# Optimization experiments

Measured on AMD Instinct MI355X. Metric: run time of the kernel, lower is better.

## Reference

```python
import jax, jax.numpy as jnp
import numpy as np

B, D_IN = 4096, 1024
E, K = 16, 2
EMB = 256
H1, H2 = 2048, 1024  # hidden_units, hidden_units // 2
O = 512              # num_classes


def setup_inputs() -> dict:
    key = jax.random.key(0)
    ks = jax.random.split(key, 10)
    s = lambda *sh: 1.0 / np.sqrt(sh[-2] if len(sh) > 1 else 1.0)
    return {
        "x":   jax.random.normal(ks[0], (B, D_IN), jnp.float32),
        "Wr":  jax.random.normal(ks[1], (D_IN, EMB), jnp.float32) * (1.0 / np.sqrt(D_IN)),
        "br":  jnp.zeros((EMB,), jnp.float32),
        "emb": jax.random.normal(ks[2], (E, EMB), jnp.float32) * (1.0 / np.sqrt(EMB)),
        "W1":  jax.random.normal(ks[3], (E, D_IN, H1), jnp.float32) * (1.0 / np.sqrt(D_IN)),
        "b1":  jnp.zeros((E, H1), jnp.float32),
        "W2":  jax.random.normal(ks[4], (E, H1, H2), jnp.float32) * (1.0 / np.sqrt(H1)),
        "b2":  jnp.zeros((E, H2), jnp.float32),
        "W3":  jax.random.normal(ks[5], (E, H2, O), jnp.float32) * (1.0 / np.sqrt(H2)),
        "b3":  jnp.zeros((E, O), jnp.float32),
    }


def reference(x, Wr, br, emb, W1, b1, W2, b2, W3, b3):
    # Router query: [B, EMB]
    q = x @ Wr + br
    # Negative squared euclidean distance to expert embeddings -> scores [B, E]
    d2 = jnp.sum(jnp.square(q[:, None, :] - emb[None, :, :]), axis=-1)
    scores = -d2
    gating_probs = jax.nn.softmax(scores, axis=-1)  # [B, E]
    # Top-k selection + renormalized gates
    top_v, top_i = jax.lax.top_k(scores, K)          # [B, K]
    gates = jax.nn.softmax(top_v, axis=-1)           # [B, K]
    # All experts run on full batch (dense), batched over expert axis
    h1 = jax.nn.relu(jnp.einsum('bi,eih->beh', x, W1) + b1)   # [B, E, H1]
    h2 = jax.nn.relu(jnp.einsum('beh,ehm->bem', h1, W2) + b2)  # [B, E, H2]
    out = jnp.einsum('bem,emo->beo', h2, W3) + b3              # [B, E, O]
    # Gather top-k expert outputs per example and combine
    sel = jnp.take_along_axis(out, top_i[:, :, None], axis=1)  # [B, K, O]
    final = jnp.sum(sel * gates[:, :, None], axis=1)           # [B, O]
    return final, q, gating_probs
```

## Files before the change

### kernel.cpp

```cpp
#include <hip/hip_runtime.h>
#include <hip/hip_bf16.h>

using bf16 = __hip_bfloat16;
typedef __attribute__((ext_vector_type(8))) short bf16x8;
typedef __attribute__((ext_vector_type(8))) unsigned short u16x8;
typedef __attribute__((ext_vector_type(4))) float f32x4;

constexpr int BATCH = 4096;
constexpr int D_IN  = 1024;
constexpr int NEXP  = 16;
constexpr int EMB   = 256;
constexpr int H1    = 2048;
constexpr int H2    = 1024;
constexpr int OUTD  = 512;
constexpr int SLOTS = BATCH * 2;
constexpr int SLOTS_PAD = SLOTS + 256;
constexpr int MAX_T128 = SLOTS / 128 + NEXP;
constexpr int K3    = 3 * D_IN;

constexpr size_t WS_XB     = 0;
constexpr size_t WS_XLO    = WS_XB     + (size_t)BATCH * D_IN * 2;
constexpr size_t WS_H1     = WS_XLO    + (size_t)BATCH * D_IN * 2;
constexpr size_t WS_H2     = WS_H1     + (size_t)SLOTS_PAD * H1 * 2;
constexpr size_t WS_OSL    = WS_H2     + (size_t)SLOTS_PAD * H2 * 2;
constexpr size_t WS_TOPI   = WS_OSL    + (size_t)SLOTS_PAD * OUTD * 4;
constexpr size_t WS_GATES  = WS_TOPI   + (size_t)SLOTS * 4;
constexpr size_t WS_SLOTOF = WS_GATES  + (size_t)SLOTS * 4;
constexpr size_t WS_TOKL   = WS_SLOTOF + (size_t)SLOTS * 4;
constexpr size_t WS_CNT    = WS_TOKL   + (size_t)SLOTS_PAD * 4;
constexpr size_t WS_TMAP   = WS_CNT    + 64 * 4;
constexpr size_t WS_WR3    = ((WS_TMAP + (size_t)MAX_T128 * 8) + 255) & ~(size_t)255;
constexpr size_t WS_WT     = ((WS_WR3 + (size_t)EMB * K3 * 2) + 255) & ~(size_t)255;

__device__ __forceinline__ unsigned short f2bf(float f) {
    bf16 h = __float2bfloat16(f);
    return __builtin_bit_cast(unsigned short, h);
}
__device__ __forceinline__ float bf2f(unsigned short h) {
    return __builtin_bit_cast(float, (unsigned)h << 16);
}

__device__ __forceinline__ void gload16(const unsigned short* g, unsigned short* l) {
    __builtin_amdgcn_global_load_lds(
        (const __attribute__((address_space(1))) unsigned int*)g,
        (__attribute__((address_space(3))) unsigned int*)l, 16, 0, 0);
}

template <int N>
__device__ __forceinline__ void waitcnt_vm() {
    if constexpr (N == 0)       asm volatile("s_waitcnt vmcnt(0)" ::: "memory");
    else if constexpr (N == 4)  asm volatile("s_waitcnt vmcnt(4)" ::: "memory");
    else if constexpr (N == 6)  asm volatile("s_waitcnt vmcnt(6)" ::: "memory");
    else if constexpr (N == 8)  asm volatile("s_waitcnt vmcnt(8)" ::: "memory");
    else if constexpr (N == 12) asm volatile("s_waitcnt vmcnt(12)" ::: "memory");
    else if constexpr (N == 16) asm volatile("s_waitcnt vmcnt(16)" ::: "memory");
    else static_assert(N == 0, "add case");
}

__global__ __launch_bounds__(256) void k_cvt_x(const float* __restrict__ x,
                                               unsigned short* __restrict__ xhi,
                                               unsigned short* __restrict__ xlo) {
    int i = blockIdx.x * 256 + threadIdx.x;
    float4 v = reinterpret_cast<const float4*>(x)[i];
    ushort4 h, l;
    h.x = f2bf(v.x); h.y = f2bf(v.y); h.z = f2bf(v.z); h.w = f2bf(v.w);
    l.x = f2bf(v.x - bf2f(h.x)); l.y = f2bf(v.y - bf2f(h.y));
    l.z = f2bf(v.z - bf2f(h.z)); l.w = f2bf(v.w - bf2f(h.w));
    reinterpret_cast<ushort4*>(xhi)[i] = h;
    reinterpret_cast<ushort4*>(xlo)[i] = l;
}

__global__ __launch_bounds__(256) void k_wr3(const float* __restrict__ Wr,
                                             unsigned short* __restrict__ Wrt3) {
    __shared__ float Tf[64][65];
    int n0 = blockIdx.x * 64, k0 = blockIdx.y * 64;
    const float* Wb = Wr + (size_t)k0 * EMB + n0;
    int t  = threadIdx.x;
    int kr = t >> 4, c4 = (t & 15) * 4;
#pragma unroll
    for (int i = 0; i < 4; i++) {
        float4 v = *reinterpret_cast<const float4*>(Wb + (size_t)(kr + i * 16) * EMB + c4);
        Tf[kr + i * 16][c4 + 0] = v.x; Tf[kr + i * 16][c4 + 1] = v.y;
        Tf[kr + i * 16][c4 + 2] = v.z; Tf[kr + i * 16][c4 + 3] = v.w;
    }
    __syncthreads();
#pragma unroll
    for (int i = 0; i < 2; i++) {
        int idx = t + i * 256;
        int n = idx >> 3, ck = (idx & 7) * 8;
        u16x8 hi, lo;
#pragma unroll
        for (int j = 0; j < 8; j++) {
            float w = Tf[ck + j][n];
            unsigned short h = f2bf(w);
            hi[j] = h; lo[j] = f2bf(w - bf2f(h));
        }
        unsigned short* dst = Wrt3 + (size_t)(n0 + n) * K3 + k0 + ck;
        *reinterpret_cast<u16x8*>(dst)            = hi;
        *reinterpret_cast<u16x8*>(dst + D_IN)     = hi;
        *reinterpret_cast<u16x8*>(dst + 2 * D_IN) = lo;
    }
}

__global__ __launch_bounds__(256) void k_wtrans(const float* __restrict__ W,
                                                unsigned short* __restrict__ Wt,
                                                int KD, int ND) {
    __shared__ float Tf[64][65];
    int e = blockIdx.z;
    int n0 = blockIdx.x * 64, k0 = blockIdx.y * 64;
    const float* Wb = W + ((size_t)e * KD + k0) * ND + n0;
    int t  = threadIdx.x;
    int kr = t >> 4, c4 = (t & 15) * 4;
#pragma unroll
    for (int i = 0; i < 4; i++) {
        float4 v = *reinterpret_cast<const float4*>(Wb + (size_t)(kr + i * 16) * ND + c4);
        Tf[kr + i * 16][c4 + 0] = v.x; Tf[kr + i * 16][c4 + 1] = v.y;
        Tf[kr + i * 16][c4 + 2] = v.z; Tf[kr + i * 16][c4 + 3] = v.w;
    }
    __syncthreads();
    unsigned short* Wtb = Wt + ((size_t)e * ND + n0) * KD + k0;
#pragma unroll
    for (int i = 0; i < 2; i++) {
        int idx = t + i * 256;
        int n = idx >> 3, ck = (idx & 7) * 8;
        u16x8 o;
#pragma unroll
        for (int j = 0; j < 8; j++) o[j] = f2bf(Tf[ck + j][n]);
        *reinterpret_cast<u16x8*>(Wtb + (size_t)n * KD + ck) = o;
    }
}

__global__ __launch_bounds__(256) void k_router3(const unsigned short* __restrict__ xhi,
                                                 const unsigned short* __restrict__ xlo,
                                                 const unsigned short* __restrict__ wrt3,
                                                 const float* __restrict__ br,
                                                 float* __restrict__ qout) {
    int nb = blockIdx.x * 64;
    int mb = blockIdx.y * 64;

    __shared__ __align__(16) unsigned short As[2][64 * 64];
    __shared__ __align__(16) unsigned short Bs[2][64 * 64];

    int t    = threadIdx.x;
    int lane = t & 63;
    int w    = t >> 6;
    int wr   = (w >> 1) * 32;
    int wc   = (w & 1) * 32;

    int srow = t >> 3;
    int swz  = (t & 7) ^ (srow & 7);
    size_t aoff[2], boff[2];
#pragma unroll
    for (int i = 0; i < 2; i++) {
        int row = i * 32 + srow;
        aoff[i] = (size_t)(mb + row) * D_IN + swz * 8;
        boff[i] = (size_t)(nb + row) * K3 + swz * 8;
    }

    auto STAGE = [&](int buf, int tts) {
        const unsigned short* abase = (tts >= 16 && tts < 32) ? xlo : xhi;
        int kk = (tts & 15) * 64;
#pragma unroll
        for (int i = 0; i < 2; i++) {
            gload16(abase + aoff[i] + kk, &As[buf][(i * 32 + w * 8) * 64] + lane * 8);
            gload16(wrt3 + boff[i] + tts * 64, &Bs[buf][(i * 32 + w * 8) * 64] + lane * 8);
        }
    };

    f32x4 acc[2][2];
#pragma unroll
    for (int mi = 0; mi < 2; mi++)
#pragma unroll
        for (int ni = 0; ni < 2; ni++) acc[mi][ni] = {0.f, 0.f, 0.f, 0.f};

    int lr  = lane & 15;
    int lkc = lane >> 4;

    constexpr int NT = K3 / 64;
    STAGE(0, 0);
    STAGE(1, 1);

    for (int tt = 0; tt < NT; tt++) {
        int cur = tt & 1;
        if (tt + 1 < NT) waitcnt_vm<4>(); else waitcnt_vm<0>();
        __builtin_amdgcn_s_barrier();
        const char* Ab = (const char*)As[cur];
        const char* Bb = (const char*)Bs[cur];
#pragma unroll
        for (int ks = 0; ks < 2; ks++) {
            bf16x8 a[2], b[2];
#pragma unroll
            for (int mi = 0; mi < 2; mi++) {
                int row = wr + mi * 16 + lr;
                int c   = (lkc + ks * 4) ^ (row & 7);
                a[mi] = *reinterpret_cast<const bf16x8*>(Ab + row * 128 + c * 16);
            }
#pragma unroll
            for (int ni = 0; ni < 2; ni++) {
                int row = wc + ni * 16 + lr;
                int c   = (lkc + ks * 4) ^ (row & 7);
                b[ni] = *reinterpret_cast<const bf16x8*>(Bb + row * 128 + c * 16);
            }
#pragma unroll
            for (int mi = 0; mi < 2; mi++)
#pragma unroll
                for (int ni = 0; ni < 2; ni++)
                    acc[mi][ni] = __builtin_amdgcn_mfma_f32_16x16x32_bf16(a[mi], b[ni], acc[mi][ni], 0, 0, 0);
        }
        __builtin_amdgcn_s_barrier();
        if (tt + 2 < NT) STAGE(cur, tt + 2);
    }

    int rowbase = (lane >> 4) * 4;
#pragma unroll
    for (int ni = 0; ni < 2; ni++) {
        int col = nb + wc + ni * 16 + lr;
        float bv = br[col];
#pragma unroll
        for (int mi = 0; mi < 2; mi++) {
#pragma unroll
            for (int qi = 0; qi < 4; qi++) {
                int row = mb + wr + mi * 16 + rowbase + qi;
                qout[(size_t)row * EMB + col] = acc[mi][ni][qi] + bv;
            }
        }
    }
}

__global__ __launch_bounds__(256) void k_router_topk(const float* __restrict__ q,
                                                     const float* __restrict__ emb,
                                                     float* __restrict__ gp,
                                                     int* __restrict__ topi,
                                                     float* __restrict__ gates) {
    int b    = blockIdx.x * 4 + (threadIdx.x >> 6);
    int lane = threadIdx.x & 63;
    int e    = lane & 15;
    int seg  = (lane >> 4) * 64;
    const float* qr = q + (size_t)b * EMB + seg;
    const float* er = emb + (size_t)e * EMB + seg;
    float d2 = 0.f;
#pragma unroll 8
    for (int i = 0; i < 64; i++) { float d = qr[i] - er[i]; d2 = fmaf(d, d, d2); }
    d2 += __shfl_xor(d2, 16);
    d2 += __shfl_xor(d2, 32);
    float s = -d2;
    float m = s;
#pragma unroll
    for (int o = 1; o < 16; o <<= 1) m = fmaxf(m, __shfl_xor(m, o));
    float ex  = __expf(s - m);
    float sum = ex;
#pragma unroll
    for (int o = 1; o < 16; o <<= 1) sum += __shfl_xor(sum, o);
    if (lane < 16) gp[(size_t)b * NEXP + lane] = ex / sum;
    float v1 = s; int i1 = e;
#pragma unroll
    for (int o = 1; o < 16; o <<= 1) {
        float ov = __shfl_xor(v1, o); int oi = __shfl_xor(i1, o);
        if (ov > v1 || (ov == v1 && oi < i1)) { v1 = ov; i1 = oi; }
    }
    float s2 = (e == i1) ? -1e30f : s;
    float v2 = s2; int i2 = e;
#pragma unroll
    for (int o = 1; o < 16; o <<= 1) {
        float ov = __shfl_xor(v2, o); int oi = __shfl_xor(i2, o);
        if (ov > v2 || (ov == v2 && oi < i2)) { v2 = ov; i2 = oi; }
    }
    if (lane == 0) {
        topi[b * 2] = i1; topi[b * 2 + 1] = i2;
        float tv  = __expf(v2 - v1);
        float inv = 1.f / (1.f + tv);
        gates[b * 2] = inv; gates[b * 2 + 1] = tv * inv;
    }
}

__global__ void k_zero(int* counts) { if (threadIdx.x < NEXP) counts[threadIdx.x] = 0; }

__global__ __launch_bounds__(256) void k_count(const int* __restrict__ topi, int* __restrict__ counts) {
    int i = blockIdx.x * 256 + threadIdx.x;
    atomicAdd(&counts[topi[i]], 1);
}

__global__ void k_scan(const int* __restrict__ counts, int* __restrict__ offsets,
                       int* __restrict__ cursors, int2* __restrict__ tmap) {
    if (threadIdx.x != 0) return;
    int off = 0;
    for (int e = 0; e < NEXP; e++) {
        offsets[e] = off; cursors[e] = off;
        off += counts[e];
    }
    int nt = 0;
    for (int e = 0; e < NEXP; e++) {
        int c = counts[e];
        for (int base = 0; base < c; base += 128) tmap[nt++] = make_int2(e, base);
    }
    for (; nt < MAX_T128; nt++) tmap[nt] = make_int2(-1, 0);
}

__global__ __launch_bounds__(256) void k_scatter(const int* __restrict__ topi, int* __restrict__ cursors,
                                                 int* __restrict__ toklist, int* __restrict__ slotof) {
    int i = blockIdx.x * 256 + threadIdx.x;
    int e = topi[i];
    int s = atomicAdd(&cursors[e], 1);
    toklist[s] = i >> 1;
    slotof[i]  = s;
}

template <int KD, int ND, int WN, int MODE>
__global__ __launch_bounds__(WN * 64, 2) void k_gemm(
    const unsigned short* __restrict__ Xin, const unsigned short* __restrict__ Wt,
    const float* __restrict__ bg, unsigned short* __restrict__ Hout,
    float* __restrict__ Oout, const int* __restrict__ counts,
    const int* __restrict__ offsets, const int* __restrict__ toklist,
    const int2* __restrict__ tmap) {
    constexpr int THREADS = WN * 64;
    constexpr int BM = 128;
    constexpr int BN = WN * 64;
    constexpr int FM = 8;
    constexpr int FN = 4;
    constexpr int RPI   = THREADS / 8;
    constexpr int A_ISS = (BM / 2) / RPI;
    constexpr int B_ISS = (BN / 2) / RPI;
    constexpr int SL    = A_ISS + B_ISS;

    int2 tm = tmap[blockIdx.y];
    int e = tm.x;
    if (e < 0) return;
    int base = tm.y;
    int n_e  = counts[e];
    int off  = offsets[e];
    int n0   = blockIdx.x * BN;

    __shared__ __align__(16) unsigned short As[3][(BM / 2) * 64];
    __shared__ __align__(16) unsigned short Bs[3][(BN / 2) * 64];

    int t    = threadIdx.x;
    int lane = t & 63;
    int w    = t >> 6;
    int wn   = w;

    int srow  = t >> 3;
    int chunk = t & 7;
    const unsigned short* asrc[A_ISS];
    const unsigned short* bsrc[B_ISS];
#pragma unroll
    for (int i = 0; i < A_ISS; i++) {
        int r  = i * RPI + srow;
        int js = chunk ^ (r & 7);
        int m_local = 2 * r + (js >> 2);
        int koff    = (js & 3) * 8;
        int g = base + m_local;
        size_t arow;
        if (MODE == 0) {
            int gg = (g < n_e) ? g : (n_e - 1);
            arow = (size_t)toklist[off + gg];
        } else {
            arow = (size_t)(off + g);
        }
        asrc[i] = Xin + arow * KD + koff;
    }
#pragma unroll
    for (int i = 0; i < B_ISS; i++) {
        int r  = i * RPI + srow;
        int js = chunk ^ (r & 7);
        int n_local = 2 * r + (js >> 2);
        int koff    = (js & 3) * 8;
        bsrc[i] = Wt + ((size_t)e * ND + n0 + n_local) * KD + koff;
    }

    auto STAGE = [&](int buf, int kt) {
#pragma unroll
        for (int i = 0; i < A_ISS; i++)
            gload16(asrc[i] + kt, &As[buf][(i * RPI + w * 8) * 64] + lane * 8);
#pragma unroll
        for (int i = 0; i < B_ISS; i++)
            gload16(bsrc[i] + kt, &Bs[buf][(i * RPI + w * 8) * 64] + lane * 8);
    };

    f32x4 acc[FM][FN];
#pragma unroll
    for (int mi = 0; mi < FM; mi++)
#pragma unroll
        for (int ni = 0; ni < FN; ni++) acc[mi][ni] = {0.f, 0.f, 0.f, 0.f};

    int lr  = lane & 15;
    int lkc = lane >> 4;
    int jrd    = (((lr & 1) << 2) + lkc) ^ ((lr >> 1) & 7);
    int abase_ = (lr >> 1) * 128 + jrd * 16;
    int bbase_ = wn * 4096 + (lr >> 1) * 128 + jrd * 16;

    constexpr int NT = KD / 32;
    STAGE(0, 0);
    STAGE(1, 32);
    STAGE(2, 64);

    int cur = 0;
    for (int tt = 0; tt < NT; tt++) {
        if (tt + 2 < NT)      waitcnt_vm<2 * SL>();
        else if (tt + 1 < NT) waitcnt_vm<SL>();
        else                  waitcnt_vm<0>();
        __builtin_amdgcn_s_barrier();
        const char* Ab = (const char*)As[cur];
        const char* Bb = (const char*)Bs[cur];
        bf16x8 a[FM], b[FN];
#pragma unroll
        for (int ni = 0; ni < FN; ni++)
            b[ni] = *reinterpret_cast<const bf16x8*>(Bb + bbase_ + ni * 1024);
#pragma unroll
        for (int mi = 0; mi < FM; mi++)
            a[mi] = *reinterpret_cast<const bf16x8*>(Ab + abase_ + mi * 1024);
#pragma unroll
        for (int mi = 0; mi < FM; mi++)
#pragma unroll
            for (int ni = 0; ni < FN; ni++)
                acc[mi][ni] = __builtin_amdgcn_mfma_f32_16x16x32_bf16(a[mi], b[ni], acc[mi][ni], 0, 0, 0);
        __builtin_amdgcn_s_barrier();
        if (tt + 3 < NT) STAGE(cur, (tt + 3) * 32);
        cur = (cur == 2) ? 0 : cur + 1;
    }

    int rowbase = (lane >> 4) * 4;
#pragma unroll
    for (int ni = 0; ni < FN; ni++) {
        int col = n0 + wn * 64 + ni * 16 + lr;
        float bv = bg[(size_t)e * ND + col];
#pragma unroll
        for (int mi = 0; mi < FM; mi++) {
#pragma unroll
            for (int qi = 0; qi < 4; qi++) {
                int g = base + mi * 16 + rowbase + qi;
                if (g < n_e) {
                    float v = acc[mi][ni][qi] + bv;
                    if (MODE == 2) {
                        Oout[(size_t)(off + g) * ND + col] = v;
                    } else {
                        v = fmaxf(v, 0.f);
                        Hout[(size_t)(off + g) * ND + col] = f2bf(v);
                    }
                }
            }
        }
    }
}

__global__ __launch_bounds__(128) void k_combine(const float* __restrict__ osl,
                                                 const float* __restrict__ gates,
                                                 const int* __restrict__ slotof,
                                                 float* __restrict__ outf) {
    int b = blockIdx.x;
    int j = threadIdx.x;
    int s0 = slotof[b * 2], s1 = slotof[b * 2 + 1];
    float g0 = gates[b * 2], g1 = gates[b * 2 + 1];
    float4 o0 = reinterpret_cast<const float4*>(osl + (size_t)s0 * OUTD)[j];
    float4 o1 = reinterpret_cast<const float4*>(osl + (size_t)s1 * OUTD)[j];
    float4 r;
    r.x = g0 * o0.x + g1 * o1.x;
    r.y = g0 * o0.y + g1 * o1.y;
    r.z = g0 * o0.z + g1 * o1.z;
    r.w = g0 * o0.w + g1 * o1.w;
    reinterpret_cast<float4*>(outf + (size_t)b * OUTD)[j] = r;
}

extern "C" void kernel_launch(void* const* d_in, const int* in_sizes, int n_in,
                              void* d_out, int out_size, void* d_ws, size_t ws_size,
                              hipStream_t stream) {
    const float* x   = (const float*)d_in[0];
    const float* Wr  = (const float*)d_in[1];
    const float* br  = (const float*)d_in[2];
    const float* emb = (const float*)d_in[3];
    const float* W1  = (const float*)d_in[4];
    const float* b1  = (const float*)d_in[5];
    const float* W2  = (const float*)d_in[6];
    const float* b2  = (const float*)d_in[7];
    const float* W3  = (const float*)d_in[8];
    const float* b3  = (const float*)d_in[9];

    float* out_final = (float*)d_out;
    float* out_q     = out_final + (size_t)BATCH * OUTD;
    float* out_gp    = out_q + (size_t)BATCH * EMB;

    char* ws = (char*)d_ws;
    unsigned short* xb  = (unsigned short*)(ws + WS_XB);
    unsigned short* xlo = (unsigned short*)(ws + WS_XLO);
    unsigned short* h1  = (unsigned short*)(ws + WS_H1);
    unsigned short* h2  = (unsigned short*)(ws + WS_H2);
    float* osl    = (float*)(ws + WS_OSL);
    int*   topi   = (int*)(ws + WS_TOPI);
    float* gates  = (float*)(ws + WS_GATES);
    int*   slotof = (int*)(ws + WS_SLOTOF);
    int*   toklist= (int*)(ws + WS_TOKL);
    int*   counts = (int*)(ws + WS_CNT);
    int*   offsets= counts + 16;
    int*   cursors= counts + 32;
    int2*  tmap   = (int2*)(ws + WS_TMAP);
    unsigned short* wrt3 = (unsigned short*)(ws + WS_WR3);
    unsigned short* wt   = (unsigned short*)(ws + WS_WT);

    k_cvt_x<<<BATCH * D_IN / 4 / 256, 256, 0, stream>>>(x, xb, xlo);
    k_wr3<<<dim3(EMB / 64, D_IN / 64), 256, 0, stream>>>(Wr, wrt3);
    k_router3<<<dim3(EMB / 64, BATCH / 64), 256, 0, stream>>>(xb, xlo, wrt3, br, out_q);
    k_router_topk<<<BATCH / 4, 256, 0, stream>>>(out_q, emb, out_gp, topi, gates);
    k_zero<<<1, 64, 0, stream>>>(counts);
    k_count<<<SLOTS / 256, 256, 0, stream>>>(topi, counts);
    k_scan<<<1, 64, 0, stream>>>(counts, offsets, cursors, tmap);
    k_scatter<<<SLOTS / 256, 256, 0, stream>>>(topi, cursors, toklist, slotof);

    k_wtrans<<<dim3(H1 / 64, D_IN / 64, NEXP), 256, 0, stream>>>(W1, wt, D_IN, H1);
    k_gemm<D_IN, H1, 4, 0><<<dim3(H1 / 256, MAX_T128), 256, 0, stream>>>(
        xb, wt, b1, h1, nullptr, counts, offsets, toklist, tmap);

    k_wtrans<<<dim3(H2 / 64, H1 / 64, NEXP), 256, 0, stream>>>(W2, wt, H1, H2);
    k_gemm<H1, H2, 4, 1><<<dim3(H2 / 256, MAX_T128), 256, 0, stream>>>(
        h1, wt, b2, h2, nullptr, counts, offsets, toklist, tmap);

    k_wtrans<<<dim3(OUTD / 64, H2 / 64, NEXP), 256, 0, stream>>>(W3, wt, H2, OUTD);
    k_gemm<H2, OUTD, 4, 2><<<dim3(OUTD / 256, MAX_T128), 256, 0, stream>>>(
        h2, wt, b3, nullptr, osl, counts, offsets, toklist, tmap);

    k_combine<<<BATCH, 128, 0, stream>>>(osl, gates, slotof, out_final);
}
```

Measured before the change: 400.9 us.

## Overlap weight transposes with GEMMs via horizontal kernel fusion and double-buffered weights

Merges the x conversion, router weight preparation and counter zeroing into one prep launch. The W1 transpose moves into the router GEMM launch, and each expert GEMM launch also carries the transpose blocks for the next layer's weights. Expert counting is folded into the top-k kernel. The goal is fewer launches and letting the memory-bound transposes fill idle CUs during the small grouped GEMMs. It needs a second weight workspace buffer and falls back to a serial path when the workspace is too small; the mixed block roles may unbalance scheduling or reduce occupancy.

```diff
diff --git a/kernel.cpp b/kernel.cpp
--- a/kernel.cpp
+++ b/kernel.cpp
@@ -31,6 +31,9 @@
 constexpr size_t WS_TMAP   = WS_CNT    + 64 * 4;
 constexpr size_t WS_WR3    = ((WS_TMAP + (size_t)MAX_T128 * 8) + 255) & ~(size_t)255;
 constexpr size_t WS_WT     = ((WS_WR3 + (size_t)EMB * K3 * 2) + 255) & ~(size_t)255;
+constexpr size_t WT_BYTES  = (size_t)NEXP * H1 * D_IN * 2;
+constexpr size_t WS_WTB    = WS_WT + WT_BYTES;
+constexpr size_t WS_NEED_FUSED = WS_WTB + WT_BYTES;
 
 __device__ __forceinline__ unsigned short f2bf(float f) {
     bf16 h = __float2bfloat16(f);
@@ -53,69 +56,22 @@
     else if constexpr (N == 6)  asm volatile("s_waitcnt vmcnt(6)" ::: "memory");
     else if constexpr (N == 8)  asm volatile("s_waitcnt vmcnt(8)" ::: "memory");
     else if constexpr (N == 12) asm volatile("s_waitcnt vmcnt(12)" ::: "memory");
-    else if constexpr (N == 16) asm volatile("s_waitcnt vmcnt(16)" ::: "memory");
     else static_assert(N == 0, "add case");
 }
 
-__global__ __launch_bounds__(256) void k_cvt_x(const float* __restrict__ x,
-                                               unsigned short* __restrict__ xhi,
-                                               unsigned short* __restrict__ xlo) {
-    int i = blockIdx.x * 256 + threadIdx.x;
-    float4 v = reinterpret_cast<const float4*>(x)[i];
-    ushort4 h, l;
-    h.x = f2bf(v.x); h.y = f2bf(v.y); h.z = f2bf(v.z); h.w = f2bf(v.w);
-    l.x = f2bf(v.x - bf2f(h.x)); l.y = f2bf(v.y - bf2f(h.y));
-    l.z = f2bf(v.z - bf2f(h.z)); l.w = f2bf(v.w - bf2f(h.w));
-    reinterpret_cast<ushort4*>(xhi)[i] = h;
-    reinterpret_cast<ushort4*>(xlo)[i] = l;
-}
-
-__global__ __launch_bounds__(256) void k_wr3(const float* __restrict__ Wr,
-                                             unsigned short* __restrict__ Wrt3) {
-    __shared__ float Tf[64][65];
-    int n0 = blockIdx.x * 64, k0 = blockIdx.y * 64;
-    const float* Wb = Wr + (size_t)k0 * EMB + n0;
+__device__ __forceinline__ void wtrans_body(const float* __restrict__ W,
+                                            unsigned short* __restrict__ Wt,
+                                            int KD, int ND, int e, int k0, int n0,
+                                            char* smem) {
+    float* Tf = (float*)smem;
     int t  = threadIdx.x;
     int kr = t >> 4, c4 = (t & 15) * 4;
-#pragma unroll
-    for (int i = 0; i < 4; i++) {
-        float4 v = *reinterpret_cast<const float4*>(Wb + (size_t)(kr + i * 16) * EMB + c4);
-        Tf[kr + i * 16][c4 + 0] = v.x; Tf[kr + i * 16][c4 + 1] = v.y;
-        Tf[kr + i * 16][c4 + 2] = v.z; Tf[kr + i * 16][c4 + 3] = v.w;
-    }
-    __syncthreads();
-#pragma unroll
-    for (int i = 0; i < 2; i++) {
-        int idx = t + i * 256;
-        int n = idx >> 3, ck = (idx & 7) * 8;
-        u16x8 hi, lo;
-#pragma unroll
-        for (int j = 0; j < 8; j++) {
-            float w = Tf[ck + j][n];
-            unsigned short h = f2bf(w);
-            hi[j] = h; lo[j] = f2bf(w - bf2f(h));
-        }
-        unsigned short* dst = Wrt3 + (size_t)(n0 + n) * K3 + k0 + ck;
-        *reinterpret_cast<u16x8*>(dst)            = hi;
-        *reinterpret_cast<u16x8*>(dst + D_IN)     = hi;
-        *reinterpret_cast<u16x8*>(dst + 2 * D_IN) = lo;
-    }
-}
-
-__global__ __launch_bounds__(256) void k_wtrans(const float* __restrict__ W,
-                                                unsigned short* __restrict__ Wt,
-                                                int KD, int ND) {
-    __shared__ float Tf[64][65];
-    int e = blockIdx.z;
-    int n0 = blockIdx.x * 64, k0 = blockIdx.y * 64;
     const float* Wb = W + ((size_t)e * KD + k0) * ND + n0;
-    int t  = threadIdx.x;
-    int kr = t >> 4, c4 = (t & 15) * 4;
 #pragma unroll
     for (int i = 0; i < 4; i++) {
         float4 v = *reinterpret_cast<const float4*>(Wb + (size_t)(kr + i * 16) * ND + c4);
-        Tf[kr + i * 16][c4 + 0] = v.x; Tf[kr + i * 16][c4 + 1] = v.y;
-        Tf[kr + i * 16][c4 + 2] = v.z; Tf[kr + i * 16][c4 + 3] = v.w;
+        Tf[(kr + i * 16) * 65 + c4 + 0] = v.x; Tf[(kr + i * 16) * 65 + c4 + 1] = v.y;
+        Tf[(kr + i * 16) * 65 + c4 + 2] = v.z; Tf[(kr + i * 16) * 65 + c4 + 3] = v.w;
     }
     __syncthreads();
     unsigned short* Wtb = Wt + ((size_t)e * ND + n0) * KD + k0;
@@ -125,21 +81,83 @@
         int n = idx >> 3, ck = (idx & 7) * 8;
         u16x8 o;
 #pragma unroll
-        for (int j = 0; j < 8; j++) o[j] = f2bf(Tf[ck + j][n]);
+        for (int j = 0; j < 8; j++) o[j] = f2bf(Tf[(ck + j) * 65 + n]);
         *reinterpret_cast<u16x8*>(Wtb + (size_t)n * KD + ck) = o;
     }
 }
 
-__global__ __launch_bounds__(256) void k_router3(const unsigned short* __restrict__ xhi,
-                                                 const unsigned short* __restrict__ xlo,
-                                                 const unsigned short* __restrict__ wrt3,
-                                                 const float* __restrict__ br,
-                                                 float* __restrict__ qout) {
-    int nb = blockIdx.x * 64;
-    int mb = blockIdx.y * 64;
-
-    __shared__ __align__(16) unsigned short As[2][64 * 64];
-    __shared__ __align__(16) unsigned short Bs[2][64 * 64];
+__global__ __launch_bounds__(256) void k_prep(const float* __restrict__ x,
+                                              unsigned short* __restrict__ xhi,
+                                              unsigned short* __restrict__ xlo,
+                                              const float* __restrict__ Wr,
+                                              unsigned short* __restrict__ Wrt3,
+                                              int* __restrict__ counts) {
+    __shared__ float Tf[64][65];
+    int bx = blockIdx.x, t = threadIdx.x;
+    if (bx < 4096) {
+        int i = bx * 256 + t;
+        float4 v = reinterpret_cast<const float4*>(x)[i];
+        ushort4 h, l;
+        h.x = f2bf(v.x); h.y = f2bf(v.y); h.z = f2bf(v.z); h.w = f2bf(v.w);
+        l.x = f2bf(v.x - bf2f(h.x)); l.y = f2bf(v.y - bf2f(h.y));
+        l.z = f2bf(v.z - bf2f(h.z)); l.w = f2bf(v.w - bf2f(h.w));
+        reinterpret_cast<ushort4*>(xhi)[i] = h;
+        reinterpret_cast<ushort4*>(xlo)[i] = l;
+    } else if (bx < 4160) {
+        int idx = bx - 4096;
+        int n0 = (idx & 3) * 64, k0 = (idx >> 2) * 64;
+        const float* Wb = Wr + (size_t)k0 * EMB + n0;
+        int kr = t >> 4, c4 = (t & 15) * 4;
+#pragma unroll
+        for (int i = 0; i < 4; i++) {
+            float4 v = *reinterpret_cast<const float4*>(Wb + (size_t)(kr + i * 16) * EMB + c4);
+            Tf[kr + i * 16][c4 + 0] = v.x; Tf[kr + i * 16][c4 + 1] = v.y;
+            Tf[kr + i * 16][c4 + 2] = v.z; Tf[kr + i * 16][c4 + 3] = v.w;
+        }
+        __syncthreads();
+#pragma unroll
+        for (int i = 0; i < 2; i++) {
+            int idx2 = t + i * 256;
+            int n = idx2 >> 3, ck = (idx2 & 7) * 8;
+            u16x8 hi, lo;
+#pragma unroll
+            for (int j = 0; j < 8; j++) {
+                float w = Tf[ck + j][n];
+                unsigned short h = f2bf(w);
+                hi[j] = h; lo[j] = f2bf(w - bf2f(h));
+            }
+            unsigned short* dst = Wrt3 + (size_t)(n0 + n) * K3 + k0 + ck;
+            *reinterpret_cast<u16x8*>(dst)            = hi;
+            *reinterpret_cast<u16x8*>(dst + D_IN)     = hi;
+            *reinterpret_cast<u16x8*>(dst + 2 * D_IN) = lo;
+        }
+    } else {
+        if (t < 16) counts[t] = 0;
+    }
+}
+
+__global__ __launch_bounds__(256) void k_router_wt1(const unsigned short* __restrict__ xhi,
+                                                    const unsigned short* __restrict__ xlo,
+                                                    const unsigned short* __restrict__ wrt3,
+                                                    const float* __restrict__ br,
+                                                    float* __restrict__ qout,
+                                                    const float* __restrict__ W1,
+                                                    unsigned short* __restrict__ wt1) {
+    __shared__ __align__(16) char smem[32768];
+    int bx = blockIdx.x;
+    if (bx >= 256) {
+        int idx = bx - 256;
+        int e   = idx >> 9;
+        int rem = idx & 511;
+        int k0  = (rem >> 5) << 6;
+        int n0  = (rem & 31) << 6;
+        wtrans_body(W1, wt1, D_IN, H1, e, k0, n0, smem);
+        return;
+    }
+    unsigned short* As = (unsigned short*)smem;
+    unsigned short* Bs = As + 8192;
+    int nb = (bx & 3) * 64;
+    int mb = (bx >> 2) * 64;
 
     int t    = threadIdx.x;
     int lane = t & 63;
@@ -162,8 +180,8 @@
         int kk = (tts & 15) * 64;
 #pragma unroll
         for (int i = 0; i < 2; i++) {
-            gload16(abase + aoff[i] + kk, &As[buf][(i * 32 + w * 8) * 64] + lane * 8);
-            gload16(wrt3 + boff[i] + tts * 64, &Bs[buf][(i * 32 + w * 8) * 64] + lane * 8);
+            gload16(abase + aoff[i] + kk, As + buf * 4096 + (i * 32 + w * 8) * 64 + lane * 8);
+            gload16(wrt3 + boff[i] + tts * 64, Bs + buf * 4096 + (i * 32 + w * 8) * 64 + lane * 8);
         }
     };
 
@@ -184,8 +202,8 @@
         int cur = tt & 1;
         if (tt + 1 < NT) waitcnt_vm<4>(); else waitcnt_vm<0>();
         __builtin_amdgcn_s_barrier();
-        const char* Ab = (const char*)As[cur];
-        const char* Bb = (const char*)Bs[cur];
+        const char* Ab = (const char*)(As + cur * 4096);
+        const char* Bb = (const char*)(Bs + cur * 4096);
 #pragma unroll
         for (int ks = 0; ks < 2; ks++) {
             bf16x8 a[2], b[2];
@@ -227,11 +245,12 @@
     }
 }
 
-__global__ __launch_bounds__(256) void k_router_topk(const float* __restrict__ q,
-                                                     const float* __restrict__ emb,
-                                                     float* __restrict__ gp,
-                                                     int* __restrict__ topi,
-                                                     float* __restrict__ gates) {
+__global__ __launch_bounds__(256) void k_topk_count(const float* __restrict__ q,
+                                                    const float* __restrict__ emb,
+                                                    float* __restrict__ gp,
+                                                    int* __restrict__ topi,
+                                                    float* __restrict__ gates,
+                                                    int* __restrict__ counts) {
     int b    = blockIdx.x * 4 + (threadIdx.x >> 6);
     int lane = threadIdx.x & 63;
     int e    = lane & 15;
@@ -270,14 +289,9 @@
         float tv  = __expf(v2 - v1);
         float inv = 1.f / (1.f + tv);
         gates[b * 2] = inv; gates[b * 2 + 1] = tv * inv;
-    }
-}
-
-__global__ void k_zero(int* counts) { if (threadIdx.x < NEXP) counts[threadIdx.x] = 0; }
-
-__global__ __launch_bounds__(256) void k_count(const int* __restrict__ topi, int* __restrict__ counts) {
-    int i = blockIdx.x * 256 + threadIdx.x;
-    atomicAdd(&counts[topi[i]], 1);
+        atomicAdd(&counts[i1], 1);
+        atomicAdd(&counts[i2], 1);
+    }
 }
 
 __global__ void k_scan(const int* __restrict__ counts, int* __restrict__ offsets,
@@ -305,13 +319,21 @@
     slotof[i]  = s;
 }
 
-template <int KD, int ND, int WN, int MODE>
-__global__ __launch_bounds__(WN * 64, 2) void k_gemm(
+__global__ __launch_bounds__(256) void k_wtrans(const float* __restrict__ W,
+                                                unsigned short* __restrict__ Wt,
+                                                int KD, int ND) {
+    __shared__ __align__(16) char smem[64 * 65 * 4];
+    wtrans_body(W, Wt, KD, ND, blockIdx.z, blockIdx.y * 64, blockIdx.x * 64, smem);
+}
+
+template <int KD, int ND, int WN, int MODE, int KD2, int ND2, int DO_WT>
+__global__ __launch_bounds__(WN * 64, 2) void k_gemm_wt(
     const unsigned short* __restrict__ Xin, const unsigned short* __restrict__ Wt,
     const float* __restrict__ bg, unsigned short* __restrict__ Hout,
     float* __restrict__ Oout, const int* __restrict__ counts,
     const int* __restrict__ offsets, const int* __restrict__ toklist,
-    const int2* __restrict__ tmap) {
+    const int2* __restrict__ tmap, const float* __restrict__ Wnext,
+    unsigned short* __restrict__ Wtnext) {
     constexpr int THREADS = WN * 64;
     constexpr int BM = 128;
     constexpr int BN = WN * 64;
@@ -321,17 +343,38 @@
     constexpr int A_ISS = (BM / 2) / RPI;
     constexpr int B_ISS = (BN / 2) / RPI;
     constexpr int SL    = A_ISS + B_ISS;
-
-    int2 tm = tmap[blockIdx.y];
+    constexpr int NX    = ND / BN;
+    constexpr int NB_G  = NX * MAX_T128;
+    constexpr int ABUF  = (BM / 2) * 64;
+    constexpr int BBUF  = (BN / 2) * 64;
+
+    __shared__ __align__(16) char smem[3 * (ABUF + BBUF) * 2];
+
+    int bx = blockIdx.x;
+    if (bx >= NB_G) {
+        if constexpr (DO_WT) {
+            constexpr int NBLK2 = ND2 / 64;
+            constexpr int KBLK2 = KD2 / 64;
+            int idx = bx - NB_G;
+            int e   = idx / (NBLK2 * KBLK2);
+            int rem = idx % (NBLK2 * KBLK2);
+            int k0  = (rem / NBLK2) * 64;
+            int n0  = (rem % NBLK2) * 64;
+            wtrans_body(Wnext, Wtnext, KD2, ND2, e, k0, n0, smem);
+        }
+        return;
+    }
+
+    int2 tm = tmap[bx % MAX_T128];
     int e = tm.x;
     if (e < 0) return;
     int base = tm.y;
     int n_e  = counts[e];
     int off  = offsets[e];
-    int n0   = blockIdx.x * BN;
-
-    __shared__ __align__(16) unsigned short As[3][(BM / 2) * 64];
-    __shared__ __align__(16) unsigned short Bs[3][(BN / 2) * 64];
+    int n0   = (bx / MAX_T128) * BN;
+
+    unsigned short* Asp = (unsigned short*)smem;
+    unsigned short* Bsp = Asp + 3 * ABUF;
 
     int t    = threadIdx.x;
     int lane = t & 63;
@@ -370,10 +413,10 @@
     auto STAGE = [&](int buf, int kt) {
 #pragma unroll
         for (int i = 0; i < A_ISS; i++)
-            gload16(asrc[i] + kt, &As[buf][(i * RPI + w * 8) * 64] + lane * 8);
+            gload16(asrc[i] + kt, Asp + buf * ABUF + (i * RPI + w * 8) * 64 + lane * 8);
 #pragma unroll
         for (int i = 0; i < B_ISS; i++)
-            gload16(bsrc[i] + kt, &Bs[buf][(i * RPI + w * 8) * 64] + lane * 8);
+            gload16(bsrc[i] + kt, Bsp + buf * BBUF + (i * RPI + w * 8) * 64 + lane * 8);
     };
 
     f32x4 acc[FM][FN];
@@ -399,8 +442,8 @@
         else if (tt + 1 < NT) waitcnt_vm<SL>();
         else                  waitcnt_vm<0>();
         __builtin_amdgcn_s_barrier();
-        const char* Ab = (const char*)As[cur];
-        const char* Bb = (const char*)Bs[cur];
+        const char* Ab = (const char*)(Asp + cur * ABUF);
+        const char* Bb = (const char*)(Bsp + cur * BBUF);
         bf16x8 a[FM], b[FN];
 #pragma unroll
         for (int ni = 0; ni < FN; ni++)
@@ -493,28 +536,34 @@
     int*   cursors= counts + 32;
     int2*  tmap   = (int2*)(ws + WS_TMAP);
     unsigned short* wrt3 = (unsigned short*)(ws + WS_WR3);
-    unsigned short* wt   = (unsigned short*)(ws + WS_WT);
-
-    k_cvt_x<<<BATCH * D_IN / 4 / 256, 256, 0, stream>>>(x, xb, xlo);
-    k_wr3<<<dim3(EMB / 64, D_IN / 64), 256, 0, stream>>>(Wr, wrt3);
-    k_router3<<<dim3(EMB / 64, BATCH / 64), 256, 0, stream>>>(xb, xlo, wrt3, br, out_q);
-    k_router_topk<<<BATCH / 4, 256, 0, stream>>>(out_q, emb, out_gp, topi, gates);
-    k_zero<<<1, 64, 0, stream>>>(counts);
-    k_count<<<SLOTS / 256, 256, 0, stream>>>(topi, counts);
+    unsigned short* wtA  = (unsigned short*)(ws + WS_WT);
+
+    const bool fused = (ws_size >= WS_NEED_FUSED);
+    unsigned short* wtB = fused ? (unsigned short*)(ws + WS_WTB) : wtA;
+
+    k_prep<<<4161, 256, 0, stream>>>(x, xb, xlo, Wr, wrt3, counts);
+    k_router_wt1<<<256 + 8192, 256, 0, stream>>>(xb, xlo, wrt3, br, out_q, W1, wtA);
+    k_topk_count<<<BATCH / 4, 256, 0, stream>>>(out_q, emb, out_gp, topi, gates, counts);
     k_scan<<<1, 64, 0, stream>>>(counts, offsets, cursors, tmap);
     k_scatter<<<SLOTS / 256, 256, 0, stream>>>(topi, cursors, toklist, slotof);
 
-    k_wtrans<<<dim3(H1 / 64, D_IN / 64, NEXP), 256, 0, stream>>>(W1, wt, D_IN, H1);
-    k_gemm<D_IN, H1, 4, 0><<<dim3(H1 / 256, MAX_T128), 256, 0, stream>>>(
-        xb, wt, b1, h1, nullptr, counts, offsets, toklist, tmap);
-
-    k_wtrans<<<dim3(H2 / 64, H1 / 64, NEXP), 256, 0, stream>>>(W2, wt, H1, H2);
-    k_gemm<H1, H2, 4, 1><<<dim3(H2 / 256, MAX_T128), 256, 0, stream>>>(
-        h1, wt, b2, h2, nullptr, counts, offsets, toklist, tmap);
-
-    k_wtrans<<<dim3(OUTD / 64, H2 / 64, NEXP), 256, 0, stream>>>(W3, wt, H2, OUTD);
-    k_gemm<H2, OUTD, 4, 2><<<dim3(OUTD / 256, MAX_T128), 256, 0, stream>>>(
-        h2, wt, b3, nullptr, osl, counts, offsets, toklist, tmap);
+    if (fused) {
+        k_gemm_wt<D_IN, H1, 4, 0, H1, H2, 1><<<640 + 8192, 256, 0, stream>>>(
+            xb, wtA, b1, h1, nullptr, counts, offsets, toklist, tmap, W2, wtB);
+        k_gemm_wt<H1, H2, 4, 1, H2, OUTD, 1><<<320 + 2048, 256, 0, stream>>>(
+            h1, wtB, b2, h2, nullptr, counts, offsets, toklist, tmap, W3, wtA);
+        k_gemm_wt<H2, OUTD, 4, 2, 64, 64, 0><<<160, 256, 0, stream>>>(
+            h2, wtA, b3, nullptr, osl, counts, offsets, toklist, tmap, nullptr, nullptr);
+    } else {
+        k_gemm_wt<D_IN, H1, 4, 0, 64, 64, 0><<<640, 256, 0, stream>>>(
+            xb, wtA, b1, h1, nullptr, counts, offsets, toklist, tmap, nullptr, nullptr);
+        k_wtrans<<<dim3(H2 / 64, H1 / 64, NEXP), 256, 0, stream>>>(W2, wtA, H1, H2);
+        k_gemm_wt<H1, H2, 4, 1, 64, 64, 0><<<320, 256, 0, stream>>>(
+            h1, wtA, b2, h2, nullptr, counts, offsets, toklist, tmap, nullptr, nullptr);
+        k_wtrans<<<dim3(OUTD / 64, H2 / 64, NEXP), 256, 0, stream>>>(W3, wtA, H2, OUTD);
+        k_gemm_wt<H2, OUTD, 4, 2, 64, 64, 0><<<160, 256, 0, stream>>>(
+            h2, wtA, b3, nullptr, osl, counts, offsets, toklist, tmap, nullptr, nullptr);
+    }
 
     k_combine<<<BATCH, 128, 0, stream>>>(osl, gates, slotof, out_final);
 }
```

After: 440.7 us. +9.9%, slower.
